# Optimization experiments

Hardware: AMD Instinct MI355X
Metric: run time of the kernel (lower is better)

## Reference

```python
import jax, jax.numpy as jnp
import numpy as np

N, E, C, EMB, NB, L = 20000, 640000, 64, 32, 8, 2
MAX_RADIUS = 2.5
NUM_NEIGHBORS = 32.0
RH = 32  # radial MLP hidden


def setup_inputs() -> dict:
    key = jax.random.key(0)
    ks = jax.random.split(key, 24)
    g = lambda k, shape, fan: (jax.random.normal(k, shape, dtype=jnp.float32) / np.sqrt(fan).astype(np.float32))
    inp = {
        'x': jax.random.normal(ks[0], (N, 6), dtype=jnp.float32),
        'batch': jnp.zeros((N,), dtype=jnp.int64),
        'node_attr': jax.random.randint(ks[1], (N,), 0, 100),
        'edge_src': jax.random.randint(ks[2], (E,), 0, N),
        'edge_dst': jax.random.randint(ks[3], (E,), 0, N),
        'emb_table': jax.random.normal(ks[4], (100, EMB), dtype=jnp.float32),
        'uplift_M': jax.random.normal(ks[5], (C, 2), dtype=jnp.float32),
        'h': jnp.ones((L,), jnp.float32) * 0.01,
        'mix': jnp.ones((L,), jnp.float32) * 0.5,
        'rad_W1': g(ks[6], (L, NB, RH), NB),
        'rad_b1': jnp.zeros((L, RH), jnp.float32),
        'rad_W2': g(ks[7], (L, RH, 2 * C), RH),
        'lin1_s': g(ks[8], (L, C, C), C),
        'lin1_v': g(ks[9], (L, C, C), C),
        'lin2_s': g(ks[10], (L, C, 2 * C), C),
        'lin2_v': g(ks[11], (L, C, C), C),
        'sc_s_w': g(ks[12], (L, C, EMB, 2 * C), C * EMB),
        'sc_v_w': g(ks[13], (L, C, EMB, C), C * EMB),
        'si_s': g(ks[14], (L, C, C), C),
        'si_v': g(ks[15], (L, C, C), C),
    }
    return inp


def _forward(x, batch, node_attr, edge_src, edge_dst, emb_table, uplift_M, h, mix,
             rad_W1, rad_b1, rad_W2, lin1_s, lin1_v, lin2_s, lin2_v,
             sc_s_w, sc_v_w, si_s, si_v):
    n = x.shape[0]
    emb = emb_table[node_attr]                       # [N, EMB] node embedding
    # semi-unitarize uplift matrix: Q = M (M^T M)^{-1/2} == U V^T
    U, _, Vt = jnp.linalg.svd(uplift_M, full_matrices=False)
    Q = U @ Vt                                       # [C, 2]
    xv = x.reshape(n, 2, 3)
    y_s = jnp.zeros((n, C), x.dtype)                 # hidden scalars start at 0
    y_v = jnp.einsum('nkx,ck->ncx', xv, Q)           # uplift vectors [N,C,3]
    y = (y_s, y_v)
    y_old = y
    nbas = jnp.arange(1, NB + 1, dtype=x.dtype)
    inv_nn = 1.0 / np.sqrt(NUM_NEIGHBORS).astype(np.float32)
    for i in range(L):
        pos = x[:, :3]
        ev = pos[edge_src] - pos[edge_dst]           # [E,3]
        elen = jnp.linalg.norm(ev, axis=1)
        safe = jnp.maximum(elen, 1e-9)
        sh = np.float32(np.sqrt(3.0)) * ev / safe[:, None]   # 1x1o SH, component norm
        # bessel radial basis, scaled by sqrt(NB)
        ef = (np.float32(np.sqrt(2.0 / MAX_RADIUS)) *
              jnp.sin(nbas[None, :] * jnp.pi * safe[:, None] / MAX_RADIUS) / safe[:, None])
        ef = ef * np.float32(np.sqrt(NB))
        # smooth cutoff (e3nn tetris style)
        u = 2.0 * (elen / MAX_RADIUS - 1.0)
        cut = jnp.where(u > 0, 0.0, jnp.where(u < -2, 1.0, 0.5 * (1.0 - jnp.cos(jnp.pi * u))))
        ea = cut[:, None] * sh                       # [E,3] edge attr
        # linear pre-mix
        s1 = y[0] @ lin1_s[i]                        # [N,C]
        v1 = jnp.einsum('ncx,cd->ndx', y[1], lin1_v[i])  # [N,C,3]
        # radial MLP -> per-edge TP weights
        w = jax.nn.silu(ef @ rad_W1[i] + rad_b1[i]) @ rad_W2[i]  # [E,2C]
        w1, w2 = w[:, :C], w[:, C:]
        # tensor-product messages: 0e x 1o -> 1o ; 1o . 1o -> 0e
        msg_v = (w1 * s1[edge_src])[:, :, None] * ea[:, None, :]        # [E,C,3]
        msg_s = w2 * jnp.einsum('ecx,ex->ec', v1[edge_src], ea)         # [E,C]
        agg_s = jax.ops.segment_sum(msg_s, edge_dst, num_segments=n) * inv_nn
        agg_v = jax.ops.segment_sum(msg_v, edge_dst, num_segments=n) * inv_nn
        # post linear + node-attr self connection
        out_s = agg_s @ lin2_s[i] + jnp.einsum('nc,ne,ceo->no', y[0], emb, sc_s_w[i])   # [N,2C]
        out_v = (jnp.einsum('ncx,cd->ndx', agg_v, lin2_v[i]) +
                 jnp.einsum('ncx,ne,ceo->nox', y[1], emb, sc_v_w[i]))                   # [N,C,3]
        # gated nonlinearity
        g_s = jax.nn.silu(out_s[:, :C])
        g_v = jax.nn.sigmoid(out_s[:, C:])[:, :, None] * out_v
        # self interaction
        y2_s = y[0] @ si_s[i]
        y2_v = jnp.einsum('ncx,cd->ndx', y[1], si_v[i])
        # leapfrog update
        hh = h[i] * h[i]
        m = mix[i]
        new_s = 2.0 * y[0] - y_old[0] + hh * (m * g_s + (m - 1.0) * y2_s)
        new_v = 2.0 * y[1] - y_old[1] + hh * (m * g_v + (m - 1.0) * y2_v)
        y_old = y
        y = (new_s, new_v)
        x = jnp.einsum('ncx,ck->nkx', new_v, Q).reshape(n, 6)   # project
    return x


def reference(x, batch, node_attr, edge_src, edge_dst, emb_table, uplift_M, h, mix,
              rad_W1, rad_b1, rad_W2, lin1_s, lin1_v, lin2_s, lin2_v,
              sc_s_w, sc_v_w, si_s, si_v):
    return _forward(x, batch, node_attr, edge_src, edge_dst, emb_table, uplift_M, h, mix,
                    rad_W1, rad_b1, rad_W2, lin1_s, lin1_v, lin2_s, lin2_v,
                    sc_s_w, sc_v_w, si_s, si_v)
```

## Files before the change

kernel.cpp:

```cpp
#include <hip/hip_runtime.h>
#include <cstdio>
#include <cstdint>

#define CCH 64
#define EMBD 32
#define NBD 8
#define RHD 32
#define NATTR 100
#define TBINS 64

static constexpr float MAXR    = 2.5f;
static constexpr float INVNN   = 0.17677669529663687f;
static constexpr float EFK     = 2.5298221281347035f;
static constexpr float SQRT3   = 1.7320508075688772f;
static constexpr float PI_F    = 3.14159265358979323846f;

typedef __fp16 v2h __attribute__((ext_vector_type(2)));

__device__ __forceinline__ float sigm_(float x) { return 1.f / (1.f + __expf(-x)); }
__device__ __forceinline__ float silu_(float x) { return x / (1.f + __expf(-x)); }
__device__ __forceinline__ unsigned f2bfu(float f) {
    unsigned u = __float_as_uint(f);
    return (u + 0x7FFF + ((u >> 16) & 1)) >> 16;
}
__device__ __forceinline__ unsigned pack2(float lo, float hi) {
    return f2bfu(lo) | (f2bfu(hi) << 16);
}
__device__ __forceinline__ float ulo(unsigned u) { return __uint_as_float(u << 16); }
__device__ __forceinline__ float uhi(unsigned u) { return __uint_as_float(u & 0xFFFF0000u); }
__device__ __forceinline__ v2h u2h(unsigned u) { v2h h; __builtin_memcpy(&h, &u, 4); return h; }
__device__ __forceinline__ unsigned pkh(float a, float b) {
    v2h h = __builtin_amdgcn_cvt_pkrtz(a, b);
    unsigned u; __builtin_memcpy(&u, &h, 4); return u;
}
__device__ __forceinline__ unsigned short h1(float f) {
    __fp16 h = (__fp16)f; unsigned short s; __builtin_memcpy(&s, &h, 2); return s;
}
__device__ __forceinline__ float dot2(unsigned a, unsigned b, float c) {
    return __builtin_amdgcn_fdot2(u2h(a), u2h(b), c, false);
}

__global__ void kQ(const float* M, float* Q) {
    int c = threadIdx.x;
    float m0 = M[2*c], m1 = M[2*c+1];
    float a = m0*m0, b = m0*m1, d = m1*m1;
    for (int o = 32; o > 0; o >>= 1) {
        a += __shfl_xor(a, o); b += __shfl_xor(b, o); d += __shfl_xor(d, o);
    }
    float det = a*d - b*b;
    float s = sqrtf(det);
    float t = sqrtf(a + d + 2.f*s);
    float inv = 1.f / (s*t);
    float i00 = (d + s)*inv, i01 = -b*inv, i11 = (a + s)*inv;
    Q[2*c]   = m0*i00 + m1*i01;
    Q[2*c+1] = m0*i01 + m1*i11;
}

__global__ void kRadTab(const float* __restrict__ rW1, const float* __restrict__ rb1,
                        const float* __restrict__ rW2, unsigned* __restrict__ tab) {
    int bin = blockIdx.x;
    int l   = blockIdx.y;
    int lane = threadIdx.x;
    float r = bin * (MAXR / TBINS);
    float safe = fmaxf(r, 1e-9f);
    float invSafe = 1.f / safe;
    float th = PI_F * r * (1.f / MAXR);
    float s0, c0;
    __sincosf(th, &s0, &c0);
    __shared__ float hidS[RHD];
    if (lane < RHD) {
        float hs = rb1[l*RHD + lane];
        float sPrev = 0.f, sCur = s0, twoC = 2.f*c0;
        #pragma unroll
        for (int b = 0; b < NBD; ++b) {
            float efb = EFK * sCur * invSafe;
            hs = fmaf(efb, rW1[(l*NBD + b)*RHD + lane], hs);
            float sN = fmaf(twoC, sCur, -sPrev);
            sPrev = sCur; sCur = sN;
        }
        hidS[lane] = silu_(hs);
    }
    __syncthreads();
    float w1 = 0.f, w2 = 0.f;
    #pragma unroll
    for (int rr = 0; rr < RHD; ++rr) {
        float h = hidS[rr];
        w1 = fmaf(h, rW2[(l*RHD + rr)*128 + lane], w1);
        w2 = fmaf(h, rW2[(l*RHD + rr)*128 + 64 + lane], w2);
    }
    float cut = s0*s0;
    float coef = SQRT3 * cut * invSafe;
    tab[((size_t)l*(TBINS+1) + bin)*64 + lane] = pack2(w1*coef, w2*coef);
}

__global__ void kPackW(const float* __restrict__ siv, unsigned* __restrict__ siVp) {
    int l = blockIdx.y;
    int i = blockIdx.x*256 + threadIdx.x;
    int cp = i >> 6, o = i & 63;
    siVp[l*2048 + i] = pkh(siv[l*4096 + (2*cp)*64 + o], siv[l*4096 + (2*cp+1)*64 + o]);
}

__global__ __launch_bounds__(256) void kInitLin(const float* __restrict__ x, const float* __restrict__ Qg,
        const float* __restrict__ L1v,
        float* __restrict__ yAs, float* __restrict__ yAv, float4* __restrict__ pos4,
        uint2* __restrict__ mv, int n) {
    __shared__ unsigned wPk[32*64];
    __shared__ __align__(16) unsigned bc[4][32][4];
    int t = threadIdx.x;
    for (int i = t; i < 32*64; i += 256) {
        int cp = i >> 6, o = i & 63;
        wPk[i] = pkh(L1v[(2*cp)*64 + o], L1v[(2*cp+1)*64 + o]);
    }
    __syncthreads();
    int lane = t & 63;
    int wid = t >> 6;
    float q0 = Qg[2*lane], q1 = Qg[2*lane+1];
    for (int node = blockIdx.x*4 + wid; node < n; node += gridDim.x*4) {
        const float* xr = x + (size_t)node*6;
        float x0 = xr[0], x1 = xr[1], x2 = xr[2], x3 = xr[3], x4 = xr[4], x5 = xr[5];
        float y0 = q0*x0 + q1*x3;
        float y1 = q0*x1 + q1*x4;
        float y2 = q0*x2 + q1*x5;
        float* yv = yAv + (size_t)node*192 + lane*3;
        yv[0] = y0; yv[1] = y1; yv[2] = y2;
        yAs[(size_t)node*64 + lane] = 0.f;
        if (lane == 0) pos4[node] = (float4){x0, x1, x2, 0.f};
        {
            unsigned short* p = (unsigned short*)bc[wid][lane >> 1];
            int sub = lane & 1;
            p[0*2+sub] = h1(y0); p[1*2+sub] = h1(y1); p[2*2+sub] = h1(y2);
        }
        float a0 = 0.f, a1 = 0.f, a2 = 0.f;
        #pragma unroll 8
        for (int cp = 0; cp < 32; ++cp) {
            uint4 b = *(const uint4*)&bc[wid][cp][0];
            unsigned wp = wPk[cp*64 + lane];
            a0 = dot2(b.x, wp, a0);
            a1 = dot2(b.y, wp, a1);
            a2 = dot2(b.z, wp, a2);
        }
        mv[(size_t)node*64 + lane] = (uint2){ pack2(a0, a1), pack2(a2, 0.f) };
    }
}

__global__ void kHist(const int* dst, int* cnt, int e) {
    int i = blockIdx.x*blockDim.x + threadIdx.x;
    if (i < e) atomicAdd(&cnt[dst[i]], 1);
}

__global__ void kScan(const int* cnt, int* offs, int* cursor, int n) {
    __shared__ int part[1024];
    int t = threadIdx.x;
    int chunk = (n + 1023) >> 10;
    int lo = t*chunk, hi = min(lo + chunk, n);
    int s = 0;
    for (int i = lo; i < hi; ++i) s += cnt[i];
    part[t] = s;
    __syncthreads();
    for (int o = 1; o < 1024; o <<= 1) {
        int w = (t >= o) ? part[t - o] : 0;
        __syncthreads();
        part[t] += w;
        __syncthreads();
    }
    int run = part[t] - s;
    for (int i = lo; i < hi; ++i) {
        int cv = cnt[i];
        offs[i] = run; cursor[i] = run;
        run += cv;
    }
    if (t == 1023) offs[n] = part[1023];
}

__global__ void kScatter(const int* src, const int* dst, int* cursor,
                         int* srcSorted, int e) {
    int i = blockIdx.x*blockDim.x + threadIdx.x;
    if (i < e) {
        int p = atomicAdd(&cursor[dst[i]], 1);
        srcSorted[p] = src[i];
    }
}

__global__ __launch_bounds__(256) void kT3(const float* __restrict__ embT,
        const float* __restrict__ scs, const float* __restrict__ scv,
        unsigned* __restrict__ Tsp, unsigned* __restrict__ Tvp) {
    int cp = blockIdx.x, l = blockIdx.y, ag = blockIdx.z;
    int c0 = 2*cp, c1 = c0 + 1;
    __shared__ float sS0[32*128], sS1[32*128], sV0[32*64], sV1[32*64], sE[20*EMBD];
    int t = threadIdx.x;
    const float* p0 = scs + ((size_t)(l*CCH + c0)*EMBD)*128;
    const float* p1 = scs + ((size_t)(l*CCH + c1)*EMBD)*128;
    for (int i = t; i < 32*128; i += 256) { sS0[i] = p0[i]; sS1[i] = p1[i]; }
    const float* q0 = scv + ((size_t)(l*CCH + c0)*EMBD)*64;
    const float* q1 = scv + ((size_t)(l*CCH + c1)*EMBD)*64;
    for (int i = t; i < 32*64; i += 256) { sV0[i] = q0[i]; sV1[i] = q1[i]; }
    const float* eb = embT + (size_t)ag*20*EMBD;
    for (int i = t; i < 20*EMBD; i += 256) sE[i] = eb[i];
    __syncthreads();
    if (t < 128) {
        int o = t;
        for (int a = 0; a < 20; ++a) {
            float acc0 = 0.f, acc1 = 0.f;
            #pragma unroll
            for (int e = 0; e < EMBD; ++e) {
                float ev = sE[a*EMBD + e];
                acc0 = fmaf(ev, sS0[e*128 + o], acc0);
                acc1 = fmaf(ev, sS1[e*128 + o], acc1);
            }
            int aa = ag*20 + a;
            Tsp[((size_t)(l*NATTR + aa)*32 + cp)*128 + (o & 63)*2 + (o >> 6)] = pkh(acc0, acc1);
        }
    } else if (t < 192) {
        int o = t - 128;
        for (int a = 0; a < 20; ++a) {
            float acc0 = 0.f, acc1 = 0.f;
            #pragma unroll
            for (int e = 0; e < EMBD; ++e) {
                float ev = sE[a*EMBD + e];
                acc0 = fmaf(ev, sV0[e*64 + o], acc0);
                acc1 = fmaf(ev, sV1[e*64 + o], acc1);
            }
            int aa = ag*20 + a;
            Tvp[((size_t)(l*NATTR + aa)*32 + cp)*64 + o] = pkh(acc0, acc1);
        }
    }
}

__global__ __launch_bounds__(256) void kLin1(const float* __restrict__ ys, const float* __restrict__ yv,
        const float* __restrict__ L1s, const float* __restrict__ L1v,
        uint2* __restrict__ mv, int n) {
    __shared__ uint2 wPk[32*64];
    __shared__ __align__(16) unsigned bc[4][32][4];
    int t = threadIdx.x;
    for (int i = t; i < 32*64; i += 256) {
        int cp = i >> 6, o = i & 63;
        wPk[i] = (uint2){ pkh(L1s[(2*cp)*64 + o], L1s[(2*cp+1)*64 + o]),
                          pkh(L1v[(2*cp)*64 + o], L1v[(2*cp+1)*64 + o]) };
    }
    __syncthreads();
    int lane = t & 63;
    int wid = t >> 6;
    for (int node = blockIdx.x*4 + wid; node < n; node += gridDim.x*4) {
        float ys_r = ys[(size_t)node*64 + lane];
        const float* yvp = yv + (size_t)node*192 + lane*3;
        float y0 = yvp[0], y1 = yvp[1], y2 = yvp[2];
        {
            unsigned short* p = (unsigned short*)bc[wid][lane >> 1];
            int sub = lane & 1;
            p[0*2+sub] = h1(y0); p[1*2+sub] = h1(y1);
            p[2*2+sub] = h1(y2); p[3*2+sub] = h1(ys_r);
        }
        float as = 0.f, a0 = 0.f, a1 = 0.f, a2 = 0.f;
        #pragma unroll 8
        for (int cp = 0; cp < 32; ++cp) {
            uint4 b = *(const uint4*)&bc[wid][cp][0];
            uint2 wp = wPk[cp*64 + lane];
            as = dot2(b.w, wp.x, as);
            a0 = dot2(b.x, wp.y, a0);
            a1 = dot2(b.y, wp.y, a1);
            a2 = dot2(b.z, wp.y, a2);
        }
        mv[(size_t)node*64 + lane] = (uint2){ pack2(a0, a1), pack2(a2, as) };
    }
}

template<int WITHV>
__global__ __launch_bounds__(256) void kAgg(const float4* __restrict__ pos4,
        const uint2* __restrict__ mv,
        const int* __restrict__ offs, const int* __restrict__ srcSorted,
        const unsigned* __restrict__ tabG,
        float* __restrict__ aggS, float* __restrict__ aggV, int n) {
    __shared__ unsigned tab[(TBINS+1)*64];
    __shared__ float red[4][64][4];
    int t = threadIdx.x;
    for (int i = t; i < (TBINS+1)*64; i += 256) tab[i] = tabG[i];
    __syncthreads();
    int lane = t & 63;
    int wid = t >> 6;

    for (int node = blockIdx.x; node < n; node += gridDim.x) {
        float4 pc = pos4[node];
        float px = pc.x, py = pc.y, pz = pc.z;
        int beg = offs[node], end = offs[node+1];
        float accS = 0.f, av0 = 0.f, av1 = 0.f, av2 = 0.f;
        int idx = beg + wid;
        int srcA = 0, srcB = 0;
        float4 pA = (float4){0.f,0.f,0.f,0.f};
        if (idx < end) srcA = srcSorted[idx];
        if (idx + 4 < end) srcB = srcSorted[idx + 4];
        if (idx < end) pA = pos4[srcA];
        for (; idx < end; idx += 4) {
            int srcU = srcA;
            float ex = pA.x - px, ey = pA.y - py, ez = pA.z - pz;
            srcA = srcB;
            if (idx + 8 < end) srcB = srcSorted[idx + 8];
            if (idx + 4 < end) pA = pos4[srcA];
            float el2 = ex*ex + ey*ey + ez*ez;
            if (el2 >= MAXR*MAXR) continue;
            uint2 mw = mv[(size_t)srcU*64 + lane];
            float elen = sqrtf(el2);
            float u = elen * ((float)TBINS / MAXR);
            int i0 = (int)u;
            float fr = u - (float)i0;
            unsigned t0 = tab[i0*64 + lane];
            unsigned t1 = tab[i0*64 + 64 + lane];
            float w1 = fmaf(fr, ulo(t1) - ulo(t0), ulo(t0));
            float w2 = fmaf(fr, uhi(t1) - uhi(t0), uhi(t0));
            float vv0 = ulo(mw.x), vv1 = uhi(mw.x), vv2 = ulo(mw.y);
            float dv = vv0*ex + vv1*ey + vv2*ez;
            accS = fmaf(w2, dv, accS);
            if (WITHV) {
                float tt = w1 * uhi(mw.y);
                av0 = fmaf(tt, ex, av0); av1 = fmaf(tt, ey, av1); av2 = fmaf(tt, ez, av2);
            }
        }
        red[wid][lane][0] = accS; red[wid][lane][1] = av0;
        red[wid][lane][2] = av1;  red[wid][lane][3] = av2;
        __syncthreads();
        if (wid == 0) {
            float rs = red[0][lane][0] + red[1][lane][0] + red[2][lane][0] + red[3][lane][0];
            aggS[(size_t)node*64 + lane] = rs*INVNN;
            float r0 = red[0][lane][1] + red[1][lane][1] + red[2][lane][1] + red[3][lane][1];
            float r1 = red[0][lane][2] + red[1][lane][2] + red[2][lane][2] + red[3][lane][2];
            float r2 = red[0][lane][3] + red[1][lane][3] + red[2][lane][3] + red[3][lane][3];
            float* ap = aggV + (size_t)node*192 + lane*3;
            ap[0] = r0*INVNN; ap[1] = r1*INVNN; ap[2] = r2*INVNN;
        }
        __syncthreads();
    }
}

__global__ __launch_bounds__(256) void kOutComb(const float* __restrict__ ys, const float* __restrict__ yv,
        const float* __restrict__ yolds, const float* __restrict__ yoldv,
        const float* __restrict__ aggS, const float* __restrict__ aggV, const int* __restrict__ attr,
        const float* __restrict__ L2s, const float* __restrict__ L2v,
        const unsigned* __restrict__ Tsp, const unsigned* __restrict__ Tvp,
        const float* __restrict__ siS, const unsigned* __restrict__ siVp, const float* __restrict__ Qg,
        const float* __restrict__ hArr, const float* __restrict__ mArr, int li,
        float* __restrict__ newS, float* __restrict__ newV,
        float4* __restrict__ pos4out, float* __restrict__ xout6,
        int writeY, int n) {
    __shared__ uint2 wAB[32*64];
    __shared__ uint2 wLS[32*64];
    __shared__ __align__(16) unsigned bc[4][32][8];
    int t = threadIdx.x;
    for (int i = t; i < 32*64; i += 256) {
        int cp = i >> 6, o = i & 63;
        wAB[i] = (uint2){ pkh(L2s[(2*cp)*128 + o],      L2s[(2*cp+1)*128 + o]),
                          pkh(L2s[(2*cp)*128 + 64 + o], L2s[(2*cp+1)*128 + 64 + o]) };
        wLS[i] = (uint2){ pkh(L2v[(2*cp)*64 + o], L2v[(2*cp+1)*64 + o]),
                          pkh(siS[(2*cp)*64 + o], siS[(2*cp+1)*64 + o]) };
    }
    __syncthreads();
    int lane = t & 63;
    int wid = t >> 6;
    unsigned svr[32];
    #pragma unroll
    for (int cp = 0; cp < 32; ++cp) svr[cp] = siVp[cp*64 + lane];
    float hh = hArr[li]; hh *= hh;
    float m = mArr[li];
    float q0 = Qg[2*lane], q1 = Qg[2*lane+1];
    for (int node = blockIdx.x*4 + wid; node < n; node += gridDim.x*4) {
        int a = attr[node];
        const unsigned* tS = Tsp + (size_t)a*32*128;
        const unsigned* tV = Tvp + (size_t)a*32*64;
        float as_r = aggS[(size_t)node*64 + lane];
        float ys_r = ys[(size_t)node*64 + lane];
        const float* avp = aggV + (size_t)node*192 + lane*3;
        float av0 = avp[0], av1 = avp[1], av2 = avp[2];
        const float* yvp = yv + (size_t)node*192 + lane*3;
        float by0 = yvp[0], by1 = yvp[1], by2 = yvp[2];
        {
            unsigned short* p = (unsigned short*)bc[wid][lane >> 1];
            int sub = lane & 1;
            p[0*2+sub] = h1(as_r); p[1*2+sub] = h1(ys_r);
            p[2*2+sub] = h1(av0);  p[3*2+sub] = h1(by0);
            p[4*2+sub] = h1(av1);  p[5*2+sub] = h1(by1);
            p[6*2+sub] = h1(av2);  p[7*2+sub] = h1(by2);
        }
        float oS0=0.f, oS1=0.f, ov0=0.f, ov1=0.f, ov2=0.f;
        float q2s=0.f, qv0=0.f, qv1=0.f, qv2=0.f;
        #pragma unroll 4
        for (int cp = 0; cp < 32; ++cp) {
            uint4 bA = *(const uint4*)&bc[wid][cp][0];
            uint4 bB = *(const uint4*)&bc[wid][cp][4];
            uint2 ab = wAB[cp*64 + lane];
            uint2 ls = wLS[cp*64 + lane];
            uint2 ts = *(const uint2*)&tS[(cp*64 + lane)*2];
            unsigned tv = tV[cp*64 + lane];
            oS0 = dot2(bA.x, ab.x, dot2(bA.y, ts.x, oS0));
            oS1 = dot2(bA.x, ab.y, dot2(bA.y, ts.y, oS1));
            ov0 = dot2(bA.z, ls.x, dot2(bA.w, tv, ov0));
            ov1 = dot2(bB.x, ls.x, dot2(bB.y, tv, ov1));
            ov2 = dot2(bB.z, ls.x, dot2(bB.w, tv, ov2));
            q2s = dot2(bA.y, ls.y, q2s);
            qv0 = dot2(bA.w, svr[cp], qv0);
            qv1 = dot2(bB.y, svr[cp], qv1);
            qv2 = dot2(bB.w, svr[cp], qv2);
        }
        float gs = silu_(oS0);
        float sg = sigm_(oS1);
        float gv0 = sg*ov0, gv1 = sg*ov1, gv2 = sg*ov2;
        float yos = yolds[(size_t)node*64 + lane];
        const float* yop = yoldv + (size_t)node*192 + lane*3;
        float ns  = 2.f*ys_r - yos   + hh*(m*gs  + (m-1.f)*q2s);
        float nv0 = 2.f*by0 - yop[0] + hh*(m*gv0 + (m-1.f)*qv0);
        float nv1 = 2.f*by1 - yop[1] + hh*(m*gv1 + (m-1.f)*qv1);
        float nv2 = 2.f*by2 - yop[2] + hh*(m*gv2 + (m-1.f)*qv2);
        if (writeY) {
            newS[(size_t)node*64 + lane] = ns;
            float* np = newV + (size_t)node*192 + lane*3;
            np[0] = nv0; np[1] = nv1; np[2] = nv2;
        }
        float p00 = nv0*q0, p01 = nv1*q0, p02 = nv2*q0;
        float p10 = nv0*q1, p11 = nv1*q1, p12 = nv2*q1;
        for (int o = 32; o > 0; o >>= 1) {
            p00 += __shfl_xor(p00, o); p01 += __shfl_xor(p01, o); p02 += __shfl_xor(p02, o);
            p10 += __shfl_xor(p10, o); p11 += __shfl_xor(p11, o); p12 += __shfl_xor(p12, o);
        }
        if (lane == 0) {
            if (writeY) {
                pos4out[node] = (float4){p00, p01, p02, 0.f};
            } else {
                float* xp = xout6 + (size_t)node*6;
                xp[0] = p00; xp[1] = p01; xp[2] = p02;
                xp[3] = p10; xp[4] = p11; xp[5] = p12;
            }
        }
    }
}

extern "C" void kernel_launch(void* const* d_in, const int* in_sizes, int n_in,
                              void* d_out, int out_size, void* d_ws, size_t ws_size,
                              hipStream_t stream) {
    const float* x        = (const float*)d_in[0];
    const int*   nattr    = (const int*)  d_in[2];
    const int*   esrc     = (const int*)  d_in[3];
    const int*   edst     = (const int*)  d_in[4];
    const float* embT     = (const float*)d_in[5];
    const float* upM      = (const float*)d_in[6];
    const float* hArr     = (const float*)d_in[7];
    const float* mArr     = (const float*)d_in[8];
    const float* rW1      = (const float*)d_in[9];
    const float* rb1      = (const float*)d_in[10];
    const float* rW2      = (const float*)d_in[11];
    const float* l1s      = (const float*)d_in[12];
    const float* l1v      = (const float*)d_in[13];
    const float* l2s      = (const float*)d_in[14];
    const float* l2v      = (const float*)d_in[15];
    const float* scs      = (const float*)d_in[16];
    const float* scv      = (const float*)d_in[17];
    const float* sis      = (const float*)d_in[18];
    const float* siv      = (const float*)d_in[19];
    int n = in_sizes[0] / 6;
    int e = in_sizes[3];
    float* out = (float*)d_out;

    float* w = (float*)d_ws;
    float* Q    = w; w += 128;
    float* yAs  = w; w += (size_t)n*64;
    float* yAv  = w; w += (size_t)n*192;
    float* yBs  = w; w += (size_t)n*64;
    float* yBv  = w; w += (size_t)n*192;
    float* aggS = w; w += (size_t)n*64;
    float* aggV = w; w += (size_t)n*192;
    float4* pos4 = (float4*)w; w += (size_t)n*4;
    uint2* mv    = (uint2*)w;  w += (size_t)n*128;
    unsigned* Tsp = (unsigned*)w; w += (size_t)2*NATTR*32*128;
    unsigned* Tvp = (unsigned*)w; w += (size_t)2*NATTR*32*64;
    unsigned* radTab = (unsigned*)w; w += (size_t)2*(TBINS+1)*64;
    unsigned* siVp = (unsigned*)w; w += (size_t)2*2048;
    int* cnt       = (int*)w;
    int* offs      = cnt + n;
    int* cursor    = offs + (n + 1);
    int* srcSorted = cursor + n;
    size_t need = (size_t)((char*)(srcSorted + e) - (char*)d_ws);
    if (need > ws_size) {
        fprintf(stderr, "kernel_launch: ws too small (%zu > %zu)\n", need, ws_size);
        return;
    }

    const int AGG_GRID  = 1792;
    const int OC_GRID   = 1024;
    const int LIN_GRID  = 2048;

    kQ<<<1, 64, 0, stream>>>(upM, Q);
    hipMemsetAsync(cnt, 0, (size_t)n*sizeof(int), stream);
    kHist<<<(e + 255)/256, 256, 0, stream>>>(edst, cnt, e);
    kScan<<<1, 1024, 0, stream>>>(cnt, offs, cursor, n);
    kScatter<<<(e + 255)/256, 256, 0, stream>>>(esrc, edst, cursor, srcSorted, e);
    kT3<<<dim3(32, 2, 5), 256, 0, stream>>>(embT, scs, scv, Tsp, Tvp);
    kRadTab<<<dim3(TBINS+1, 2), 64, 0, stream>>>(rW1, rb1, rW2, radTab);
    kPackW<<<dim3(8, 2), 256, 0, stream>>>(siv, siVp);
    kInitLin<<<LIN_GRID, 256, 0, stream>>>(x, Q, l1v, yAs, yAv, pos4, mv, n);

    kAgg<0><<<AGG_GRID, 256, 0, stream>>>(pos4, mv, offs, srcSorted,
                                  radTab, aggS, aggV, n);
    kOutComb<<<OC_GRID, 256, 0, stream>>>(yAs, yAv, yAs, yAv, aggS, aggV, nattr,
                                  l2s, l2v, Tsp, Tvp, sis, siVp, Q, hArr, mArr, 0,
                                  yBs, yBv, pos4, out, 1, n);
    kLin1<<<LIN_GRID, 256, 0, stream>>>(yBs, yBv, l1s + 4096, l1v + 4096, mv, n);
    kAgg<1><<<AGG_GRID, 256, 0, stream>>>(pos4, mv, offs, srcSorted,
                                  radTab + (size_t)(TBINS+1)*64, aggS, aggV, n);
    kOutComb<<<OC_GRID, 256, 0, stream>>>(yBs, yBv, yAs, yAv, aggS, aggV, nattr,
                                  l2s + (size_t)64*128, l2v + (size_t)64*64,
                                  Tsp + (size_t)NATTR*32*128, Tvp + (size_t)NATTR*32*64,
                                  sis + 4096, siVp + 2048, Q, hArr, mArr, 1,
                                  yAs, yAv, pos4, out, 0, n);
}
```

Baseline: 516.3 us.

## Precompute per-edge geometry records and interleave packed output-combine weights

```diff
diff --git a/kernel.cpp b/kernel.cpp
--- a/kernel.cpp
+++ b/kernel.cpp
@@ -39,6 +39,8 @@
 __device__ __forceinline__ float dot2(unsigned a, unsigned b, float c) {
     return __builtin_amdgcn_fdot2(u2h(a), u2h(b), c, false);
 }
+__device__ __forceinline__ float hlo(unsigned u) { v2h h = u2h(u); return (float)h.x; }
+__device__ __forceinline__ float hhi(unsigned u) { v2h h = u2h(u); return (float)h.y; }
 
 __global__ void kQ(const float* M, float* Q) {
     int c = threadIdx.x;
@@ -89,7 +91,7 @@
         w2 = fmaf(h, rW2[(l*RHD + rr)*128 + 64 + lane], w2);
     }
     float cut = s0*s0;
-    float coef = SQRT3 * cut * invSafe;
+    float coef = SQRT3 * cut * invSafe * INVNN;
     tab[((size_t)l*(TBINS+1) + bin)*64 + lane] = pack2(w1*coef, w2*coef);
 }
 
@@ -173,17 +175,37 @@
 }
 
 __global__ void kScatter(const int* src, const int* dst, int* cursor,
-                         int* srcSorted, int e) {
+                         int* srcSorted, int* dstSorted, int e) {
     int i = blockIdx.x*blockDim.x + threadIdx.x;
     if (i < e) {
-        int p = atomicAdd(&cursor[dst[i]], 1);
+        int d = dst[i];
+        int p = atomicAdd(&cursor[d], 1);
         srcSorted[p] = src[i];
-    }
+        dstSorted[p] = d;
+    }
+}
+
+__global__ __launch_bounds__(256) void kGeom(const float4* __restrict__ pos4,
+        const int* __restrict__ srcSorted, const int* __restrict__ dstSorted,
+        uint4* __restrict__ rec, int e) {
+    int i = blockIdx.x*256 + threadIdx.x;
+    if (i >= e) return;
+    int s = srcSorted[i], d = dstSorted[i];
+    float4 pa = pos4[s], pb = pos4[d];
+    float ex = pa.x - pb.x, ey = pa.y - pb.y, ez = pa.z - pb.z;
+    float el2 = ex*ex + ey*ey + ez*ez;
+    if (el2 >= MAXR*MAXR) {
+        rec[i] = (uint4){0xFFFFFFFFu, 0u, 0u, 0u};
+        return;
+    }
+    float elen = sqrtf(el2);
+    float u = fminf(elen * ((float)TBINS / MAXR), 63.98f);
+    rec[i] = (uint4){ (unsigned)s, pkh(ex, ey), pkh(ez, u), 0u };
 }
 
 __global__ __launch_bounds__(256) void kT3(const float* __restrict__ embT,
         const float* __restrict__ scs, const float* __restrict__ scv,
-        unsigned* __restrict__ Tsp, unsigned* __restrict__ Tvp) {
+        unsigned* __restrict__ TallU) {
     int cp = blockIdx.x, l = blockIdx.y, ag = blockIdx.z;
     int c0 = 2*cp, c1 = c0 + 1;
     __shared__ float sS0[32*128], sS1[32*128], sV0[32*64], sV1[32*64], sE[20*EMBD];
@@ -208,7 +230,8 @@
                 acc1 = fmaf(ev, sS1[e*128 + o], acc1);
             }
             int aa = ag*20 + a;
-            Tsp[((size_t)(l*NATTR + aa)*32 + cp)*128 + (o & 63)*2 + (o >> 6)] = pkh(acc0, acc1);
+            size_t idx = ((size_t)(l*NATTR + aa)*32 + cp)*64 + (o & 63);
+            TallU[idx*4 + (o >> 6)] = pkh(acc0, acc1);
         }
     } else if (t < 192) {
         int o = t - 128;
@@ -221,7 +244,8 @@
                 acc1 = fmaf(ev, sV1[e*64 + o], acc1);
             }
             int aa = ag*20 + a;
-            Tvp[((size_t)(l*NATTR + aa)*32 + cp)*64 + o] = pkh(acc0, acc1);
+            size_t idx = ((size_t)(l*NATTR + aa)*32 + cp)*64 + o;
+            TallU[idx*4 + 2] = pkh(acc0, acc1);
         }
     }
 }
@@ -265,9 +289,9 @@
 }
 
 template<int WITHV>
-__global__ __launch_bounds__(256) void kAgg(const float4* __restrict__ pos4,
+__global__ __launch_bounds__(256) void kAgg(const uint4* __restrict__ rec,
         const uint2* __restrict__ mv,
-        const int* __restrict__ offs, const int* __restrict__ srcSorted,
+        const int* __restrict__ offs,
         const unsigned* __restrict__ tabG,
         float* __restrict__ aggS, float* __restrict__ aggV, int n) {
     __shared__ unsigned tab[(TBINS+1)*64];
@@ -279,52 +303,57 @@
     int wid = t >> 6;
 
     for (int node = blockIdx.x; node < n; node += gridDim.x) {
-        float4 pc = pos4[node];
-        float px = pc.x, py = pc.y, pz = pc.z;
         int beg = offs[node], end = offs[node+1];
         float accS = 0.f, av0 = 0.f, av1 = 0.f, av2 = 0.f;
         int idx = beg + wid;
-        int srcA = 0, srcB = 0;
-        float4 pA = (float4){0.f,0.f,0.f,0.f};
-        if (idx < end) srcA = srcSorted[idx];
-        if (idx + 4 < end) srcB = srcSorted[idx + 4];
-        if (idx < end) pA = pos4[srcA];
-        for (; idx < end; idx += 4) {
-            int srcU = srcA;
-            float ex = pA.x - px, ey = pA.y - py, ez = pA.z - pz;
-            srcA = srcB;
-            if (idx + 8 < end) srcB = srcSorted[idx + 8];
-            if (idx + 4 < end) pA = pos4[srcA];
-            float el2 = ex*ex + ey*ey + ez*ez;
-            if (el2 >= MAXR*MAXR) continue;
-            uint2 mw = mv[(size_t)srcU*64 + lane];
-            float elen = sqrtf(el2);
-            float u = elen * ((float)TBINS / MAXR);
-            int i0 = (int)u;
-            float fr = u - (float)i0;
-            unsigned t0 = tab[i0*64 + lane];
-            unsigned t1 = tab[i0*64 + 64 + lane];
-            float w1 = fmaf(fr, ulo(t1) - ulo(t0), ulo(t0));
-            float w2 = fmaf(fr, uhi(t1) - uhi(t0), uhi(t0));
-            float vv0 = ulo(mw.x), vv1 = uhi(mw.x), vv2 = ulo(mw.y);
-            float dv = vv0*ex + vv1*ey + vv2*ez;
-            accS = fmaf(w2, dv, accS);
-            if (WITHV) {
-                float tt = w1 * uhi(mw.y);
-                av0 = fmaf(tt, ex, av0); av1 = fmaf(tt, ey, av1); av2 = fmaf(tt, ez, av2);
+        uint4 rC = (uint4){0xFFFFFFFFu,0u,0u,0u};
+        uint2 mwC = (uint2){0u,0u};
+        bool actC = false;
+        if (idx < end) {
+            rC = rec[idx];
+            actC = ((int)rC.x) >= 0;
+            if (actC) mwC = mv[(size_t)rC.x*64 + lane];
+        }
+        for (; idx < end; ) {
+            int nIdx = idx + 4;
+            uint4 rN = (uint4){0xFFFFFFFFu,0u,0u,0u};
+            uint2 mwN = (uint2){0u,0u};
+            bool actN = false;
+            if (nIdx < end) {
+                rN = rec[nIdx];
+                actN = ((int)rN.x) >= 0;
+                if (actN) mwN = mv[(size_t)rN.x*64 + lane];
             }
+            if (actC) {
+                float ex = hlo(rC.y), ey = hhi(rC.y);
+                float ez = hlo(rC.z), u = hhi(rC.z);
+                int i0 = (int)u;
+                float fr = u - (float)i0;
+                unsigned t0 = tab[i0*64 + lane];
+                unsigned t1 = tab[i0*64 + 64 + lane];
+                float w1 = fmaf(fr, ulo(t1) - ulo(t0), ulo(t0));
+                float w2 = fmaf(fr, uhi(t1) - uhi(t0), uhi(t0));
+                float vv0 = ulo(mwC.x), vv1 = uhi(mwC.x), vv2 = ulo(mwC.y);
+                float dv = vv0*ex + vv1*ey + vv2*ez;
+                accS = fmaf(w2, dv, accS);
+                if (WITHV) {
+                    float tt = w1 * uhi(mwC.y);
+                    av0 = fmaf(tt, ex, av0); av1 = fmaf(tt, ey, av1); av2 = fmaf(tt, ez, av2);
+                }
+            }
+            rC = rN; mwC = mwN; actC = actN; idx = nIdx;
         }
         red[wid][lane][0] = accS; red[wid][lane][1] = av0;
         red[wid][lane][2] = av1;  red[wid][lane][3] = av2;
         __syncthreads();
         if (wid == 0) {
             float rs = red[0][lane][0] + red[1][lane][0] + red[2][lane][0] + red[3][lane][0];
-            aggS[(size_t)node*64 + lane] = rs*INVNN;
+            aggS[(size_t)node*64 + lane] = rs;
             float r0 = red[0][lane][1] + red[1][lane][1] + red[2][lane][1] + red[3][lane][1];
             float r1 = red[0][lane][2] + red[1][lane][2] + red[2][lane][2] + red[3][lane][2];
             float r2 = red[0][lane][3] + red[1][lane][3] + red[2][lane][3] + red[3][lane][3];
             float* ap = aggV + (size_t)node*192 + lane*3;
-            ap[0] = r0*INVNN; ap[1] = r1*INVNN; ap[2] = r2*INVNN;
+            ap[0] = r0; ap[1] = r1; ap[2] = r2;
         }
         __syncthreads();
     }
@@ -334,22 +363,21 @@
         const float* __restrict__ yolds, const float* __restrict__ yoldv,
         const float* __restrict__ aggS, const float* __restrict__ aggV, const int* __restrict__ attr,
         const float* __restrict__ L2s, const float* __restrict__ L2v,
-        const unsigned* __restrict__ Tsp, const unsigned* __restrict__ Tvp,
+        const uint4* __restrict__ Tall,
         const float* __restrict__ siS, const unsigned* __restrict__ siVp, const float* __restrict__ Qg,
         const float* __restrict__ hArr, const float* __restrict__ mArr, int li,
         float* __restrict__ newS, float* __restrict__ newV,
         float4* __restrict__ pos4out, float* __restrict__ xout6,
         int writeY, int n) {
-    __shared__ uint2 wAB[32*64];
-    __shared__ uint2 wLS[32*64];
+    __shared__ uint4 wAll[32*64];
     __shared__ __align__(16) unsigned bc[4][32][8];
     int t = threadIdx.x;
     for (int i = t; i < 32*64; i += 256) {
         int cp = i >> 6, o = i & 63;
-        wAB[i] = (uint2){ pkh(L2s[(2*cp)*128 + o],      L2s[(2*cp+1)*128 + o]),
-                          pkh(L2s[(2*cp)*128 + 64 + o], L2s[(2*cp+1)*128 + 64 + o]) };
-        wLS[i] = (uint2){ pkh(L2v[(2*cp)*64 + o], L2v[(2*cp+1)*64 + o]),
-                          pkh(siS[(2*cp)*64 + o], siS[(2*cp+1)*64 + o]) };
+        wAll[i] = (uint4){ pkh(L2s[(2*cp)*128 + o],      L2s[(2*cp+1)*128 + o]),
+                           pkh(L2s[(2*cp)*128 + 64 + o], L2s[(2*cp+1)*128 + 64 + o]),
+                           pkh(L2v[(2*cp)*64 + o], L2v[(2*cp+1)*64 + o]),
+                           pkh(siS[(2*cp)*64 + o], siS[(2*cp+1)*64 + o]) };
     }
     __syncthreads();
     int lane = t & 63;
@@ -362,8 +390,7 @@
     float q0 = Qg[2*lane], q1 = Qg[2*lane+1];
     for (int node = blockIdx.x*4 + wid; node < n; node += gridDim.x*4) {
         int a = attr[node];
-        const unsigned* tS = Tsp + (size_t)a*32*128;
-        const unsigned* tV = Tvp + (size_t)a*32*64;
+        const uint4* tA = Tall + (size_t)a*2048;
         float as_r = aggS[(size_t)node*64 + lane];
         float ys_r = ys[(size_t)node*64 + lane];
         const float* avp = aggV + (size_t)node*192 + lane*3;
@@ -384,16 +411,14 @@
         for (int cp = 0; cp < 32; ++cp) {
             uint4 bA = *(const uint4*)&bc[wid][cp][0];
             uint4 bB = *(const uint4*)&bc[wid][cp][4];
-            uint2 ab = wAB[cp*64 + lane];
-            uint2 ls = wLS[cp*64 + lane];
-            uint2 ts = *(const uint2*)&tS[(cp*64 + lane)*2];
-            unsigned tv = tV[cp*64 + lane];
-            oS0 = dot2(bA.x, ab.x, dot2(bA.y, ts.x, oS0));
-            oS1 = dot2(bA.x, ab.y, dot2(bA.y, ts.y, oS1));
-            ov0 = dot2(bA.z, ls.x, dot2(bA.w, tv, ov0));
-            ov1 = dot2(bB.x, ls.x, dot2(bB.y, tv, ov1));
-            ov2 = dot2(bB.z, ls.x, dot2(bB.w, tv, ov2));
-            q2s = dot2(bA.y, ls.y, q2s);
+            uint4 wv4 = wAll[cp*64 + lane];
+            uint4 tw  = tA[cp*64 + lane];
+            oS0 = dot2(bA.x, wv4.x, dot2(bA.y, tw.x, oS0));
+            oS1 = dot2(bA.x, wv4.y, dot2(bA.y, tw.y, oS1));
+            ov0 = dot2(bA.z, wv4.z, dot2(bA.w, tw.z, ov0));
+            ov1 = dot2(bB.x, wv4.z, dot2(bB.y, tw.z, ov1));
+            ov2 = dot2(bB.z, wv4.z, dot2(bB.w, tw.z, ov2));
+            q2s = dot2(bA.y, wv4.w, q2s);
             qv0 = dot2(bA.w, svr[cp], qv0);
             qv1 = dot2(bB.y, svr[cp], qv1);
             qv2 = dot2(bB.w, svr[cp], qv2);
@@ -466,15 +491,16 @@
     float* aggV = w; w += (size_t)n*192;
     float4* pos4 = (float4*)w; w += (size_t)n*4;
     uint2* mv    = (uint2*)w;  w += (size_t)n*128;
-    unsigned* Tsp = (unsigned*)w; w += (size_t)2*NATTR*32*128;
-    unsigned* Tvp = (unsigned*)w; w += (size_t)2*NATTR*32*64;
+    uint4* Tall  = (uint4*)w;  w += (size_t)2*NATTR*2048*4;
     unsigned* radTab = (unsigned*)w; w += (size_t)2*(TBINS+1)*64;
     unsigned* siVp = (unsigned*)w; w += (size_t)2*2048;
+    uint4* rec = (uint4*)w; w += (size_t)e*4;
     int* cnt       = (int*)w;
     int* offs      = cnt + n;
     int* cursor    = offs + (n + 1);
     int* srcSorted = cursor + n;
-    size_t need = (size_t)((char*)(srcSorted + e) - (char*)d_ws);
+    int* dstSorted = srcSorted + e;
+    size_t need = (size_t)((char*)(dstSorted + e) - (char*)d_ws);
     if (need > ws_size) {
         fprintf(stderr, "kernel_launch: ws too small (%zu > %zu)\n", need, ws_size);
         return;
@@ -483,28 +509,30 @@
     const int AGG_GRID  = 1792;
     const int OC_GRID   = 1024;
     const int LIN_GRID  = 2048;
+    int eb = (e + 255)/256;
 
     kQ<<<1, 64, 0, stream>>>(upM, Q);
     hipMemsetAsync(cnt, 0, (size_t)n*sizeof(int), stream);
-    kHist<<<(e + 255)/256, 256, 0, stream>>>(edst, cnt, e);
+    kHist<<<eb, 256, 0, stream>>>(edst, cnt, e);
     kScan<<<1, 1024, 0, stream>>>(cnt, offs, cursor, n);
-    kScatter<<<(e + 255)/256, 256, 0, stream>>>(esrc, edst, cursor, srcSorted, e);
-    kT3<<<dim3(32, 2, 5), 256, 0, stream>>>(embT, scs, scv, Tsp, Tvp);
+    kScatter<<<eb, 256, 0, stream>>>(esrc, edst, cursor, srcSorted, dstSorted, e);
+    kT3<<<dim3(32, 2, 5), 256, 0, stream>>>(embT, scs, scv, (unsigned*)Tall);
     kRadTab<<<dim3(TBINS+1, 2), 64, 0, stream>>>(rW1, rb1, rW2, radTab);
     kPackW<<<dim3(8, 2), 256, 0, stream>>>(siv, siVp);
     kInitLin<<<LIN_GRID, 256, 0, stream>>>(x, Q, l1v, yAs, yAv, pos4, mv, n);
 
-    kAgg<0><<<AGG_GRID, 256, 0, stream>>>(pos4, mv, offs, srcSorted,
-                                  radTab, aggS, aggV, n);
+    kGeom<<<eb, 256, 0, stream>>>(pos4, srcSorted, dstSorted, rec, e);
+    kAgg<0><<<AGG_GRID, 256, 0, stream>>>(rec, mv, offs, radTab, aggS, aggV, n);
     kOutComb<<<OC_GRID, 256, 0, stream>>>(yAs, yAv, yAs, yAv, aggS, aggV, nattr,
-                                  l2s, l2v, Tsp, Tvp, sis, siVp, Q, hArr, mArr, 0,
+                                  l2s, l2v, Tall, sis, siVp, Q, hArr, mArr, 0,
                                   yBs, yBv, pos4, out, 1, n);
     kLin1<<<LIN_GRID, 256, 0, stream>>>(yBs, yBv, l1s + 4096, l1v + 4096, mv, n);
-    kAgg<1><<<AGG_GRID, 256, 0, stream>>>(pos4, mv, offs, srcSorted,
+    kGeom<<<eb, 256, 0, stream>>>(pos4, srcSorted, dstSorted, rec, e);
+    kAgg<1><<<AGG_GRID, 256, 0, stream>>>(rec, mv, offs,
                                   radTab + (size_t)(TBINS+1)*64, aggS, aggV, n);
     kOutComb<<<OC_GRID, 256, 0, stream>>>(yBs, yBv, yAs, yAv, aggS, aggV, nattr,
                                   l2s + (size_t)64*128, l2v + (size_t)64*64,
-                                  Tsp + (size_t)NATTR*32*128, Tvp + (size_t)NATTR*32*64,
+                                  Tall + (size_t)NATTR*2048,
                                   sis + 4096, siVp + 2048, Q, hArr, mArr, 1,
                                   yAs, yAv, pos4, out, 0, n);
 }
```

New measurement: 534.0 us. 3.4% more time.
